# Performance work log

Hardware: AMD Instinct MI355X
Metric: run time of the kernel (lower is better)

The kernel has to match this reference:

```python
import jax, jax.numpy as jnp
import numpy as np

N_NODES = 100000
N_EDGES = 3200000
N_FEAT = 512
N_DIMS = 64
N_CLSS = 10


def setup_inputs() -> dict:
    key = jax.random.key(0)
    ks = jax.random.split(key, 8)
    x = jax.random.normal(ks[0], (N_NODES, N_FEAT), dtype=jnp.float32)
    edge_index = jax.random.randint(ks[1], (2, N_EDGES), 0, N_NODES, dtype=jnp.int64)
    edge_weight = jax.random.uniform(ks[2], (N_EDGES,), dtype=jnp.float32)
    W1 = jax.random.normal(ks[3], (N_FEAT, N_DIMS), dtype=jnp.float32) * (1.0 / np.sqrt(N_FEAT))
    M1 = jax.random.normal(ks[4], (N_FEAT, N_DIMS), dtype=jnp.float32)
    b1 = jnp.zeros((N_DIMS,), dtype=jnp.float32)
    W2 = jax.random.normal(ks[5], (N_DIMS, N_CLSS), dtype=jnp.float32) * (1.0 / np.sqrt(N_DIMS))
    M2 = jax.random.normal(ks[6], (N_DIMS, N_CLSS), dtype=jnp.float32)
    b2 = jnp.zeros((N_CLSS,), dtype=jnp.float32)
    return {"x": x, "edge_index": edge_index, "edge_weight": edge_weight,
            "W1": W1, "M1": M1, "b1": b1, "W2": W2, "M2": M2, "b2": b2}


def _gcn_conv(x, edge_index, edge_weight, W, M, b):
    # MaskedGCNConv: weight = W * mask, then standard GCN symmetric-normalized propagation.
    N = x.shape[0]
    h = x @ (W * M)  # [N, n_dims]  transform-first (in_feat > out_feat)
    # add self-loops with weight 1 (GCNConv default)
    loop = jnp.arange(N, dtype=edge_index.dtype)
    src = jnp.concatenate([edge_index[0], loop])
    dst = jnp.concatenate([edge_index[1], loop])
    w = jnp.concatenate([edge_weight, jnp.ones((N,), dtype=edge_weight.dtype)])
    deg = jax.ops.segment_sum(w, dst, num_segments=N)  # in-degree with weights
    deg_inv_sqrt = jnp.where(deg > 0, jax.lax.rsqrt(jnp.maximum(deg, 1e-12)), 0.0)
    norm = deg_inv_sqrt[src] * w * deg_inv_sqrt[dst]  # [E+N]
    out = jax.ops.segment_sum(h[src] * norm[:, None], dst, num_segments=N)
    return out + b


def reference(x, edge_index, edge_weight, W1, M1, b1, W2, M2, b2):
    h = jax.nn.relu(_gcn_conv(x, edge_index, edge_weight, W1, M1, b1))
    # F.dropout(training=self.training): identity in eval mode
    logits = h @ (W2 * M2) + b2  # MaskedLinear classifier
    return logits
```

## Files before the change

### kernel.cpp

```cpp
#include <hip/hip_runtime.h>

#define NN 100000
#define NE 3200000
#define NF 512
#define ND 64
#define NC 10

#define NBUCK 196
#define NPB 500
#define EPB 6400

#define OFF_H      0
#define OFF_DIS    6400000
#define OFF_W1     6500000
#define OFF_GH     6533408
#define OFF_RP     6633408
#define OFF_BSUM   6733409
#define OFF_EDGE   6733922
#define OFF_W2F    13133922

typedef __attribute__((ext_vector_type(8))) short v8s;
typedef __attribute__((ext_vector_type(4))) float v4f;

__device__ __forceinline__ unsigned short bf16_rne(float f) {
  unsigned int u = __float_as_uint(f);
  return (unsigned short)((u + 0x7fffu + ((u >> 16) & 1u)) >> 16);
}

__global__ __launch_bounds__(256) void prep_kernel(
    const float* __restrict__ W1, const float* __restrict__ M1,
    const float* __restrict__ W2, const float* __restrict__ M2,
    float* __restrict__ ws) {
  const int i = blockIdx.x * 256 + threadIdx.x;
  if (i < NF * ND) {
    const float v = W1[i] * M1[i];
    const int k = i >> 6, d = i & 63;
    const int s = k >> 5, g = (k >> 3) & 3, e = k & 7;
    const int t = d >> 4;
    const int lane = (g << 4) | (d & 15);
    unsigned short* bp = (unsigned short*)(ws + OFF_W1);
    const int base = ((s * 4 + t) * 64 + lane) * 16 + e;
    const unsigned short hb = bf16_rne(v);
    bp[base] = hb;
    bp[base + 8] = bf16_rne(v - __uint_as_float((unsigned int)hb << 16));
  }
  if (i < ND * 16) {
    const int k = i >> 4, c = i & 15;
    const float v = (c < NC) ? W2[k * NC + c] * M2[k * NC + c] : 0.0f;
    const int s = k >> 5, g = (k >> 3) & 3, e = k & 7;
    const int lane = (g << 4) | c;
    unsigned short* bp = (unsigned short*)(ws + OFF_W2F);
    const int base = (s * 64 + lane) * 16 + e;
    const unsigned short hb = bf16_rne(v);
    bp[base] = hb;
    bp[base + 8] = bf16_rne(v - __uint_as_float((unsigned int)hb << 16));
  }
}


__global__ __launch_bounds__(256) void part_hist(
    const int* __restrict__ dst, int* __restrict__ GH) {
  __shared__ int hist[NBUCK];
  const int tid = threadIdx.x;
  for (int i = tid; i < NBUCK; i += 256) hist[i] = 0;
  __syncthreads();
  const int s0 = blockIdx.x * EPB;
  for (int e = s0 + tid; e < s0 + EPB; e += 256)
    atomicAdd(&hist[dst[e] >> 9], 1);
  __syncthreads();
  for (int i = tid; i < NBUCK; i += 256)
    GH[i * NPB + blockIdx.x] = hist[i];
}

__global__ __launch_bounds__(512) void part_scan(
    int* __restrict__ GH, int* __restrict__ T) {
  __shared__ int s[512];
  const int t = threadIdx.x;
  const int b = blockIdx.x;
  const int v = (t < NPB) ? GH[b * NPB + t] : 0;
  s[t] = v; __syncthreads();
  for (int off = 1; off < 512; off <<= 1) {
    const int a = (t >= off) ? s[t - off] : 0;
    __syncthreads();
    s[t] += a;
    __syncthreads();
  }
  if (t < NPB) GH[b * NPB + t] = s[t] - v;
  if (t == 511) T[b] = s[511];
}

__global__ __launch_bounds__(256) void part_scan_t(
    const int* __restrict__ T, int* __restrict__ TS) {
  __shared__ int s[256];
  const int t = threadIdx.x;
  const int v = (t < NBUCK) ? T[t] : 0;
  s[t] = v; __syncthreads();
  for (int off = 1; off < 256; off <<= 1) {
    const int a = (t >= off) ? s[t - off] : 0;
    __syncthreads();
    s[t] += a;
    __syncthreads();
  }
  if (t < NBUCK) TS[t] = s[t] - v;
  if (t == NBUCK - 1) TS[NBUCK] = s[t];
}

__global__ __launch_bounds__(256) void part_scatter(
    const int* __restrict__ src, const int* __restrict__ dst,
    const float* __restrict__ ew, const int* __restrict__ GH,
    const int* __restrict__ TS, int2* __restrict__ buck) {
  __shared__ int cursor[NBUCK];
  const int tid = threadIdx.x;
  for (int i = tid; i < NBUCK; i += 256)
    cursor[i] = GH[i * NPB + blockIdx.x] + TS[i];
  __syncthreads();
  const int s0 = blockIdx.x * EPB;
  for (int e = s0 + tid; e < s0 + EPB; e += 256) {
    const int d = dst[e];
    const int pos = atomicAdd(&cursor[d >> 9], 1);
    buck[pos] = make_int2(src[e] | ((d & 511) << 17), __float_as_int(ew[e]));
  }
}

__global__ __launch_bounds__(512) void bucket_sort(
    const int* __restrict__ TS, const int2* __restrict__ buck,
    int2* __restrict__ edge, int* __restrict__ rowptr,
    float* __restrict__ dis) {
  __shared__ int hist[512];
  __shared__ float deg[512];
  __shared__ int scn[512];
  const int t = threadIdx.x;
  const int b = blockIdx.x;
  const int beg = TS[b], endd = TS[b + 1];
  hist[t] = 0; deg[t] = 0.0f;
  __syncthreads();
  for (int e = beg + t; e < endd; e += 512) {
    const int2 q = buck[e];
    const int fine = (q.x >> 17) & 511;
    atomicAdd(&hist[fine], 1);
    atomicAdd(&deg[fine], __int_as_float(q.y));
  }
  __syncthreads();
  const int sv = hist[t];
  scn[t] = sv; __syncthreads();
  for (int off = 1; off < 512; off <<= 1) {
    const int a = (t >= off) ? scn[t - off] : 0;
    __syncthreads();
    scn[t] += a;
    __syncthreads();
  }
  const int ex = scn[t] - sv;
  const int node = b * 512 + t;
  if (node < NN) {
    rowptr[node] = beg + ex;
    dis[node] = rsqrtf(deg[t] + 1.0f);
  }
  if (b == NBUCK - 1 && t == 0) rowptr[NN] = endd;
  hist[t] = beg + ex;
  __syncthreads();
  for (int e = beg + t; e < endd; e += 512) {
    const int2 q = buck[e];
    const int fine = (q.x >> 17) & 511;
    const int pos = atomicAdd(&hist[fine], 1);
    edge[pos] = make_int2(q.x & 0x1FFFF, q.y);
  }
}

__global__ __launch_bounds__(256) void gemm1_kernel(
    const float* __restrict__ x, const float* __restrict__ bfrag_f,
    const float* __restrict__ dis, float* __restrict__ h) {
  const int lane = threadIdx.x & 63;
  const int wid  = threadIdx.x >> 6;
  const size_t row0 = ((size_t)blockIdx.x * 4 + wid) * 32;
  if (row0 >= NN) return;
  const int lr = lane & 15;
  const int lg = lane >> 4;
  const float* x0 = x + (row0 + lr) * NF + lg * 8;
  const v8s* bfr = (const v8s*)bfrag_f + (size_t)lane * 2;
  v4f acc[2][4];
#pragma unroll
  for (int i = 0; i < 2; ++i)
#pragma unroll
    for (int t = 0; t < 4; ++t) acc[i][t] = (v4f){0.f, 0.f, 0.f, 0.f};

  for (int s = 0; s < 16; ++s) {
    v8s ah[2], al[2];
#pragma unroll
    for (int i = 0; i < 2; ++i) {
      const float* xp = x0 + (size_t)i * (16 * NF) + s * 32;
      const float4 p0 = *(const float4*)xp;
      const float4 p1 = *(const float4*)(xp + 4);
      const float vv[8] = {p0.x, p0.y, p0.z, p0.w, p1.x, p1.y, p1.z, p1.w};
#pragma unroll
      for (int e = 0; e < 8; ++e) {
        const unsigned short hb = bf16_rne(vv[e]);
        ah[i][e] = (short)hb;
        al[i][e] = (short)bf16_rne(vv[e] - __uint_as_float((unsigned int)hb << 16));
      }
    }
#pragma unroll
    for (int t = 0; t < 4; ++t) {
      const v8s bh = bfr[(size_t)(s * 4 + t) * 128];
      const v8s bl = bfr[(size_t)(s * 4 + t) * 128 + 1];
#pragma unroll
      for (int i = 0; i < 2; ++i) {
        acc[i][t] = __builtin_amdgcn_mfma_f32_16x16x32_bf16(ah[i], bh, acc[i][t], 0, 0, 0);
        acc[i][t] = __builtin_amdgcn_mfma_f32_16x16x32_bf16(ah[i], bl, acc[i][t], 0, 0, 0);
        acc[i][t] = __builtin_amdgcn_mfma_f32_16x16x32_bf16(al[i], bh, acc[i][t], 0, 0, 0);
      }
    }
  }
#pragma unroll
  for (int i = 0; i < 2; ++i)
#pragma unroll
    for (int r = 0; r < 4; ++r) {
      const size_t row = row0 + i * 16 + lg * 4 + r;
      const float dv = dis[row];
#pragma unroll
      for (int t = 0; t < 4; ++t)
        h[row * ND + t * 16 + lr] = acc[i][t][r] * dv;
    }
}

__global__ __launch_bounds__(256) void gather_kernel(
    const int* __restrict__ rowptr, const int2* __restrict__ edge,
    const float* __restrict__ h, const float* __restrict__ dis,
    const float* __restrict__ b1, const float* __restrict__ w2f,
    const float* __restrict__ b2, float* __restrict__ out) {
  __shared__ float vls[4 * 64];
  const int lane = threadIdx.x & 63;
  const int wid  = threadIdx.x >> 6;
  const int n = blockIdx.x * 4 + wid;
  const int beg = __builtin_amdgcn_readfirstlane(rowptr[n]);
  const int end = __builtin_amdgcn_readfirstlane(rowptr[n + 1]);
  float a0 = 0.f, a1 = 0.f, a2 = 0.f, a3 = 0.f,
        a4 = 0.f, a5 = 0.f, a6 = 0.f, a7 = 0.f;
  int e = beg;
  for (; e + 8 <= end; e += 8) {
    const int2 q0 = edge[e],     q1 = edge[e + 1];
    const int2 q2 = edge[e + 2], q3 = edge[e + 3];
    const int2 q4 = edge[e + 4], q5 = edge[e + 5];
    const int2 q6 = edge[e + 6], q7 = edge[e + 7];
    a0 = fmaf(h[(size_t)q0.x * ND + lane], __int_as_float(q0.y), a0);
    a1 = fmaf(h[(size_t)q1.x * ND + lane], __int_as_float(q1.y), a1);
    a2 = fmaf(h[(size_t)q2.x * ND + lane], __int_as_float(q2.y), a2);
    a3 = fmaf(h[(size_t)q3.x * ND + lane], __int_as_float(q3.y), a3);
    a4 = fmaf(h[(size_t)q4.x * ND + lane], __int_as_float(q4.y), a4);
    a5 = fmaf(h[(size_t)q5.x * ND + lane], __int_as_float(q5.y), a5);
    a6 = fmaf(h[(size_t)q6.x * ND + lane], __int_as_float(q6.y), a6);
    a7 = fmaf(h[(size_t)q7.x * ND + lane], __int_as_float(q7.y), a7);
  }
  for (; e + 4 <= end; e += 4) {
    const int2 q0 = edge[e],     q1 = edge[e + 1];
    const int2 q2 = edge[e + 2], q3 = edge[e + 3];
    a0 = fmaf(h[(size_t)q0.x * ND + lane], __int_as_float(q0.y), a0);
    a1 = fmaf(h[(size_t)q1.x * ND + lane], __int_as_float(q1.y), a1);
    a2 = fmaf(h[(size_t)q2.x * ND + lane], __int_as_float(q2.y), a2);
    a3 = fmaf(h[(size_t)q3.x * ND + lane], __int_as_float(q3.y), a3);
  }
  for (; e < end; ++e) {
    const int2 q = edge[e];
    a0 = fmaf(h[(size_t)q.x * ND + lane], __int_as_float(q.y), a0);
  }
  const float dn = dis[n];
  const float hn = h[(size_t)n * ND + lane];
  float vv = fmaf((((a0 + a1) + (a2 + a3)) + ((a4 + a5) + (a6 + a7))) + hn,
                  dn, b1[lane]);
  vls[wid * 64 + lane] = fmaxf(vv, 0.0f);
  __syncthreads();
  if (wid == 0) {
    const int lr = lane & 15, lg = lane >> 4;
    const v8s* bfr = (const v8s*)w2f + (size_t)lane * 2;
    v4f acc = (v4f){0.f, 0.f, 0.f, 0.f};
#pragma unroll
    for (int s = 0; s < 2; ++s) {
      v8s ah, al;
#pragma unroll
      for (int k = 0; k < 8; ++k) {
        float xv = vls[(lr & 3) * 64 + s * 32 + lg * 8 + k];
        xv = (lr < 4) ? xv : 0.0f;
        const unsigned short hb = bf16_rne(xv);
        ah[k] = (short)hb;
        al[k] = (short)bf16_rne(xv - __uint_as_float((unsigned int)hb << 16));
      }
      const v8s bh = bfr[s * 128], bl = bfr[s * 128 + 1];
      acc = __builtin_amdgcn_mfma_f32_16x16x32_bf16(ah, bh, acc, 0, 0, 0);
      acc = __builtin_amdgcn_mfma_f32_16x16x32_bf16(ah, bl, acc, 0, 0, 0);
      acc = __builtin_amdgcn_mfma_f32_16x16x32_bf16(al, bh, acc, 0, 0, 0);
    }
    if (lane < NC) {
      const float bb = b2[lane];
#pragma unroll
      for (int r = 0; r < 4; ++r)
        out[(size_t)(blockIdx.x * 4 + r) * NC + lane] = acc[r] + bb;
    }
  }
}

extern "C" void kernel_launch(void* const* d_in, const int* in_sizes, int n_in,
                              void* d_out, int out_size, void* d_ws, size_t ws_size,
                              hipStream_t stream) {
  const float* x  = (const float*)d_in[0];
  const int*   ei = (const int*)d_in[1];
  const float* ew = (const float*)d_in[2];
  const float* W1 = (const float*)d_in[3];
  const float* M1 = (const float*)d_in[4];
  const float* b1 = (const float*)d_in[5];
  const float* W2 = (const float*)d_in[6];
  const float* M2 = (const float*)d_in[7];
  const float* b2 = (const float*)d_in[8];
  float* out = (float*)d_out;
  float* ws  = (float*)d_ws;
  int*   wsi = (int*)d_ws;
  const int* src = ei;
  const int* dst = ei + NE;
  int2* buck = (int2*)(ws + OFF_H);
  int2* edge = (int2*)(wsi + OFF_EDGE);
  int*  GH   = wsi + OFF_GH;
  int*  T    = wsi + OFF_BSUM;
  int*  TS   = wsi + OFF_BSUM + 256;

  prep_kernel<<<128, 256, 0, stream>>>(W1, M1, W2, M2, ws);
  part_hist<<<NPB, 256, 0, stream>>>(dst, GH);
  part_scan<<<NBUCK, 512, 0, stream>>>(GH, T);
  part_scan_t<<<1, 256, 0, stream>>>(T, TS);
  part_scatter<<<NPB, 256, 0, stream>>>(src, dst, ew, GH, TS, buck);
  bucket_sort<<<NBUCK, 512, 0, stream>>>(TS, buck, edge, wsi + OFF_RP,
                                         ws + OFF_DIS);
  gemm1_kernel<<<(NN + 127) / 128, 256, 0, stream>>>(x, ws + OFF_W1,
                                                     ws + OFF_DIS, ws + OFF_H);
  gather_kernel<<<NN / 4, 256, 0, stream>>>(wsi + OFF_RP, edge, ws + OFF_H,
                                            ws + OFF_DIS, b1, ws + OFF_W2F, b2, out);
}
```

Measured before the change: 553.0 us.

## Stage x tiles through double-buffered swizzled LDS with register prefetch in gemm1

```diff
diff --git a/kernel.cpp b/kernel.cpp
--- a/kernel.cpp
+++ b/kernel.cpp
@@ -169,13 +169,22 @@
 __global__ __launch_bounds__(256) void gemm1_kernel(
     const float* __restrict__ x, const float* __restrict__ bfrag_f,
     const float* __restrict__ dis, float* __restrict__ h) {
-  const int lane = threadIdx.x & 63;
-  const int wid  = threadIdx.x >> 6;
-  const size_t row0 = ((size_t)blockIdx.x * 4 + wid) * 32;
-  if (row0 >= NN) return;
+  __shared__ __align__(16) float xs[2][128 * 32];
+  const int tid  = threadIdx.x;
+  const int lane = tid & 63;
+  const int wid  = tid >> 6;
+  const size_t brow = (size_t)blockIdx.x * 128;
+  const int srow = tid >> 1;
+  const int bunit = (tid & 1) * 4;
+  const int sr7 = srow & 7;
+  const size_t grow = (brow + srow < NN) ? (brow + srow) : (size_t)(NN - 1);
+  const float* gx = x + grow * NF + bunit * 4;
+  float* wrow = &xs[0][0];
+
+  const size_t row0 = brow + (size_t)wid * 32;
   const int lr = lane & 15;
   const int lg = lane >> 4;
-  const float* x0 = x + (row0 + lr) * NF + lg * 8;
+  const int crow = wid * 32;
   const v8s* bfr = (const v8s*)bfrag_f + (size_t)lane * 2;
   v4f acc[2][4];
 #pragma unroll
@@ -183,13 +192,30 @@
 #pragma unroll
     for (int t = 0; t < 4; ++t) acc[i][t] = (v4f){0.f, 0.f, 0.f, 0.f};
 
+  float4 pf[4];
+#pragma unroll
+  for (int j = 0; j < 4; ++j) pf[j] = *(const float4*)(gx + j * 4);
+
   for (int s = 0; s < 16; ++s) {
+    float* buf = &xs[s & 1][0];
+    float* wr = buf + srow * 32;
+#pragma unroll
+    for (int j = 0; j < 4; ++j)
+      *(float4*)(wr + (((bunit + j) ^ sr7) << 2)) = pf[j];
+    if (s < 15) {
+      const float* gxs = gx + (s + 1) * 32;
+#pragma unroll
+      for (int j = 0; j < 4; ++j) pf[j] = *(const float4*)(gxs + j * 4);
+    }
+    __syncthreads();
     v8s ah[2], al[2];
 #pragma unroll
     for (int i = 0; i < 2; ++i) {
-      const float* xp = x0 + (size_t)i * (16 * NF) + s * 32;
-      const float4 p0 = *(const float4*)xp;
-      const float4 p1 = *(const float4*)(xp + 4);
+      const int rl = crow + i * 16 + lr;
+      const float* rp = buf + rl * 32;
+      const int r7 = rl & 7;
+      const float4 p0 = *(const float4*)(rp + (((lg * 2) ^ r7) << 2));
+      const float4 p1 = *(const float4*)(rp + (((lg * 2 + 1) ^ r7) << 2));
       const float vv[8] = {p0.x, p0.y, p0.z, p0.w, p1.x, p1.y, p1.z, p1.w};
 #pragma unroll
       for (int e = 0; e < 8; ++e) {
@@ -209,17 +235,20 @@
         acc[i][t] = __builtin_amdgcn_mfma_f32_16x16x32_bf16(al[i], bh, acc[i][t], 0, 0, 0);
       }
     }
-  }
-#pragma unroll
-  for (int i = 0; i < 2; ++i)
-#pragma unroll
-    for (int r = 0; r < 4; ++r) {
-      const size_t row = row0 + i * 16 + lg * 4 + r;
-      const float dv = dis[row];
-#pragma unroll
-      for (int t = 0; t < 4; ++t)
-        h[row * ND + t * 16 + lr] = acc[i][t][r] * dv;
-    }
+    __syncthreads();
+  }
+  if (row0 < NN) {
+#pragma unroll
+    for (int i = 0; i < 2; ++i)
+#pragma unroll
+      for (int r = 0; r < 4; ++r) {
+        const size_t row = row0 + i * 16 + lg * 4 + r;
+        const float dv = dis[row];
+#pragma unroll
+        for (int t = 0; t < 4; ++t)
+          h[row * ND + t * 16 + lr] = acc[i][t][r] * dv;
+      }
+  }
 }
 
 __global__ __launch_bounds__(256) void gather_kernel(
```

Measured after the change: 584.8 us. 5.8% more time.

## Stage x tiles through swizzled LDS with coalesced, double-buffered loads in gemm1

Applied to the files above, without the earlier changes.

```diff
diff --git a/kernel.cpp b/kernel.cpp
--- a/kernel.cpp
+++ b/kernel.cpp
@@ -169,57 +169,107 @@
 __global__ __launch_bounds__(256) void gemm1_kernel(
     const float* __restrict__ x, const float* __restrict__ bfrag_f,
     const float* __restrict__ dis, float* __restrict__ h) {
-  const int lane = threadIdx.x & 63;
-  const int wid  = threadIdx.x >> 6;
-  const size_t row0 = ((size_t)blockIdx.x * 4 + wid) * 32;
-  if (row0 >= NN) return;
+  __shared__ __align__(16) float xs[2][64 * 32];
+  const int tid  = threadIdx.x;
+  const int lane = tid & 63;
+  const int wid  = tid >> 6;
+  const size_t brow = (size_t)blockIdx.x * 64;
+  const int srow = tid >> 2;
+  const int u0   = (tid & 3) * 2;
+  const int sr7  = srow & 7;
+  size_t grow = brow + srow;
+  if (grow >= NN) grow = NN - 1;
+  const float* gx = x + grow * NF + u0 * 4;
+
   const int lr = lane & 15;
   const int lg = lane >> 4;
-  const float* x0 = x + (row0 + lr) * NF + lg * 8;
+  const size_t row0 = brow + (size_t)wid * 16;
+  const int rl = wid * 16 + lr;
+  const int r7 = rl & 7;
   const v8s* bfr = (const v8s*)bfrag_f + (size_t)lane * 2;
-  v4f acc[2][4];
-#pragma unroll
-  for (int i = 0; i < 2; ++i)
-#pragma unroll
-    for (int t = 0; t < 4; ++t) acc[i][t] = (v4f){0.f, 0.f, 0.f, 0.f};
-
-  for (int s = 0; s < 16; ++s) {
-    v8s ah[2], al[2];
-#pragma unroll
-    for (int i = 0; i < 2; ++i) {
-      const float* xp = x0 + (size_t)i * (16 * NF) + s * 32;
-      const float4 p0 = *(const float4*)xp;
-      const float4 p1 = *(const float4*)(xp + 4);
+  v4f acc[4];
+#pragma unroll
+  for (int t = 0; t < 4; ++t) acc[t] = (v4f){0.f, 0.f, 0.f, 0.f};
+
+  float4 pA0 = *(const float4*)(gx);
+  float4 pA1 = *(const float4*)(gx + 4);
+  float4 pB0 = *(const float4*)(gx + 32);
+  float4 pB1 = *(const float4*)(gx + 36);
+
+  for (int ss = 0; ss < 8; ++ss) {
+    {
+      float* wr = &xs[0][srow * 32];
+      *(float4*)(wr + ((u0 ^ sr7) << 2))       = pA0;
+      *(float4*)(wr + (((u0 + 1) ^ sr7) << 2)) = pA1;
+      if (ss < 7) {
+        const float* g2 = gx + (2 * ss + 2) * 32;
+        pA0 = *(const float4*)(g2);
+        pA1 = *(const float4*)(g2 + 4);
+      }
+      __syncthreads();
+      const float* rp = &xs[0][rl * 32];
+      const float4 p0 = *(const float4*)(rp + (((lg * 2) ^ r7) << 2));
+      const float4 p1 = *(const float4*)(rp + (((lg * 2 + 1) ^ r7) << 2));
       const float vv[8] = {p0.x, p0.y, p0.z, p0.w, p1.x, p1.y, p1.z, p1.w};
+      v8s ah, al;
 #pragma unroll
       for (int e = 0; e < 8; ++e) {
         const unsigned short hb = bf16_rne(vv[e]);
-        ah[i][e] = (short)hb;
-        al[i][e] = (short)bf16_rne(vv[e] - __uint_as_float((unsigned int)hb << 16));
-      }
-    }
-#pragma unroll
-    for (int t = 0; t < 4; ++t) {
-      const v8s bh = bfr[(size_t)(s * 4 + t) * 128];
-      const v8s bl = bfr[(size_t)(s * 4 + t) * 128 + 1];
-#pragma unroll
-      for (int i = 0; i < 2; ++i) {
-        acc[i][t] = __builtin_amdgcn_mfma_f32_16x16x32_bf16(ah[i], bh, acc[i][t], 0, 0, 0);
-        acc[i][t] = __builtin_amdgcn_mfma_f32_16x16x32_bf16(ah[i], bl, acc[i][t], 0, 0, 0);
-        acc[i][t] = __builtin_amdgcn_mfma_f32_16x16x32_bf16(al[i], bh, acc[i][t], 0, 0, 0);
-      }
-    }
-  }
-#pragma unroll
-  for (int i = 0; i < 2; ++i)
+        ah[e] = (short)hb;
+        al[e] = (short)bf16_rne(vv[e] - __uint_as_float((unsigned int)hb << 16));
+      }
+      const int s = 2 * ss;
+#pragma unroll
+      for (int t = 0; t < 4; ++t) {
+        const v8s bh = bfr[(size_t)(s * 4 + t) * 128];
+        const v8s bl = bfr[(size_t)(s * 4 + t) * 128 + 1];
+        acc[t] = __builtin_amdgcn_mfma_f32_16x16x32_bf16(ah, bh, acc[t], 0, 0, 0);
+        acc[t] = __builtin_amdgcn_mfma_f32_16x16x32_bf16(ah, bl, acc[t], 0, 0, 0);
+        acc[t] = __builtin_amdgcn_mfma_f32_16x16x32_bf16(al, bh, acc[t], 0, 0, 0);
+      }
+    }
+    {
+      float* wr = &xs[1][srow * 32];
+      *(float4*)(wr + ((u0 ^ sr7) << 2))       = pB0;
+      *(float4*)(wr + (((u0 + 1) ^ sr7) << 2)) = pB1;
+      if (ss < 7) {
+        const float* g2 = gx + (2 * ss + 3) * 32;
+        pB0 = *(const float4*)(g2);
+        pB1 = *(const float4*)(g2 + 4);
+      }
+      __syncthreads();
+      const float* rp = &xs[1][rl * 32];
+      const float4 p0 = *(const float4*)(rp + (((lg * 2) ^ r7) << 2));
+      const float4 p1 = *(const float4*)(rp + (((lg * 2 + 1) ^ r7) << 2));
+      const float vv[8] = {p0.x, p0.y, p0.z, p0.w, p1.x, p1.y, p1.z, p1.w};
+      v8s ah, al;
+#pragma unroll
+      for (int e = 0; e < 8; ++e) {
+        const unsigned short hb = bf16_rne(vv[e]);
+        ah[e] = (short)hb;
+        al[e] = (short)bf16_rne(vv[e] - __uint_as_float((unsigned int)hb << 16));
+      }
+      const int s = 2 * ss + 1;
+#pragma unroll
+      for (int t = 0; t < 4; ++t) {
+        const v8s bh = bfr[(size_t)(s * 4 + t) * 128];
+        const v8s bl = bfr[(size_t)(s * 4 + t) * 128 + 1];
+        acc[t] = __builtin_amdgcn_mfma_f32_16x16x32_bf16(ah, bh, acc[t], 0, 0, 0);
+        acc[t] = __builtin_amdgcn_mfma_f32_16x16x32_bf16(ah, bl, acc[t], 0, 0, 0);
+        acc[t] = __builtin_amdgcn_mfma_f32_16x16x32_bf16(al, bh, acc[t], 0, 0, 0);
+      }
+    }
+  }
+  if (row0 < NN) {
 #pragma unroll
     for (int r = 0; r < 4; ++r) {
-      const size_t row = row0 + i * 16 + lg * 4 + r;
+      const size_t row = row0 + lg * 4 + r;
       const float dv = dis[row];
 #pragma unroll
       for (int t = 0; t < 4; ++t)
-        h[row * ND + t * 16 + lr] = acc[i][t][r] * dv;
-    }
+        h[row * ND + t * 16 + lr] = acc[t][r] * dv;
+    }
+  }
 }
 
 __global__ __launch_bounds__(256) void gather_kernel(
@@ -327,8 +377,8 @@
   part_scatter<<<NPB, 256, 0, stream>>>(src, dst, ew, GH, TS, buck);
   bucket_sort<<<NBUCK, 512, 0, stream>>>(TS, buck, edge, wsi + OFF_RP,
                                          ws + OFF_DIS);
-  gemm1_kernel<<<(NN + 127) / 128, 256, 0, stream>>>(x, ws + OFF_W1,
-                                                     ws + OFF_DIS, ws + OFF_H);
+  gemm1_kernel<<<(NN + 63) / 64, 256, 0, stream>>>(x, ws + OFF_W1,
+                                                   ws + OFF_DIS, ws + OFF_H);
   gather_kernel<<<NN / 4, 256, 0, stream>>>(wsi + OFF_RP, edge, ws + OFF_H,
                                             ws + OFF_DIS, b1, ws + OFF_W2F, b2, out);
 }
```

Result: no change. 559.6 us (+1.2%).
